# Performance work log

Hardware: AMD Instinct MI355X
Metric: run time of the kernel (lower is better)

Reference implementation:

```python
import jax, jax.numpy as jnp
import numpy as np

B, N, D, H, ND = 16, 512, 768, 12, 32
DK = D // H  # 64
GRID = 11    # hard-coded 11x11 patch grid in SpatialCirclePosition.patch


def setup_inputs() -> dict:
    key = jax.random.key(0)
    ks = jax.random.split(key, 10)
    features = jax.random.normal(ks[0], (B, N, D), dtype=jnp.float32)
    boxes = jax.random.uniform(ks[1], (B, N, 4), dtype=jnp.float32)  # normalized [0,1]
    sizes_wh = jax.random.randint(ks[2], (B, 2), 512, 1024).astype(jnp.int32)
    image_sizes = jnp.concatenate([sizes_wh, sizes_wh], axis=-1)  # (B,4) = [w,h,w,h]
    s = 0.02
    Wq = jax.random.normal(ks[3], (D, D), dtype=jnp.float32) * s
    Wk = jax.random.normal(ks[4], (D, D), dtype=jnp.float32) * s
    Wv = jax.random.normal(ks[5], (D, D), dtype=jnp.float32) * s
    Wo = jax.random.normal(ks[6], (D, D), dtype=jnp.float32) * s
    bq = jnp.zeros((D,), jnp.float32); bk = jnp.zeros((D,), jnp.float32)
    bv = jnp.zeros((D,), jnp.float32); bo = jnp.zeros((D,), jnp.float32)
    gamma = jnp.ones((D,), jnp.float32); beta = jnp.zeros((D,), jnp.float32)
    dist_emb = jax.random.normal(ks[7], (ND, H), dtype=jnp.float32) * s
    return {"features": features, "boxes": boxes, "image_sizes": image_sizes,
            "Wq": Wq, "bq": bq, "Wk": Wk, "bk": bk, "Wv": Wv, "bv": bv,
            "Wo": Wo, "bo": bo, "gamma": gamma, "beta": beta, "dist_emb": dist_emb}


def _patch_bins(boxes_norm, image_sizes):
    # boxes_norm: (B,N,4) in [0,1]; image_sizes: (B,4)=[w,h,w,h] int
    sizes_f = image_sizes.astype(jnp.float32)
    boxes = boxes_norm * sizes_f[:, None, :]                       # pixel boxes
    spa = jnp.floor_divide(sizes_f[:, :2], 11.0)                   # (B,2) size_per_area
    lb = jnp.arange(GRID, dtype=jnp.float32)                       # (11,)
    hb = lb + 1.0
    wlb = lb[None, :] * spa[:, 0:1]; whb = hb[None, :] * spa[:, 0:1]   # (B,11)
    hlb = lb[None, :] * spa[:, 1:2]; hhb = hb[None, :] * spa[:, 1:2]
    cx = jnp.floor_divide(boxes[..., 0] + boxes[..., 2], 2.0)      # (B,N)
    cy = jnp.floor_divide(boxes[..., 1] + boxes[..., 3], 2.0)
    mx = (wlb[:, None, :] <= cx[..., None]) & (cx[..., None] <= whb[:, None, :])  # (B,N,11)
    my = (hlb[:, None, :] <= cy[..., None]) & (cy[..., None] <= hhb[:, None, :])
    px = jnp.argmax(mx.astype(jnp.float32), axis=-1)               # (B,N) int
    py = jnp.argmax(my.astype(jnp.float32), axis=-1)
    return px.astype(jnp.float32), py.astype(jnp.float32)


def _dist_bins(boxes_norm, image_sizes):
    px, py = _patch_bins(boxes_norm, image_sizes)
    dx = px[:, None, :] - px[:, :, None]                           # (B,N,N)
    dy = py[:, None, :] - py[:, :, None]
    dist = jnp.sqrt(dx * dx + dy * dy) * 2.0
    return dist.astype(jnp.int32)                                  # truncation == .long()


def reference(features, boxes, image_sizes, Wq, bq, Wk, bk, Wv, bv, Wo, bo, gamma, beta, dist_emb):
    # LayerNorm(d_model), eps matches torch default 1e-5
    mu = jnp.mean(features, axis=-1, keepdims=True)
    var = jnp.mean(jnp.square(features - mu), axis=-1, keepdims=True)
    x = (features - mu) * jax.lax.rsqrt(var + 1e-5) * gamma + beta

    bins = _dist_bins(boxes, image_sizes)                          # (B,N,N) int32
    dist_bias = dist_emb[bins]                                     # (B,N,N,H)
    dist_bias = jnp.transpose(dist_bias, (0, 3, 1, 2))             # (B,H,N,N)

    bsz, nq, _ = x.shape
    q = (x @ Wq.T + bq).reshape(bsz, nq, H, DK).transpose(0, 2, 1, 3)  # (B,H,N,DK)
    k = (x @ Wk.T + bk).reshape(bsz, nq, H, DK).transpose(0, 2, 1, 3)
    v = (x @ Wv.T + bv).reshape(bsz, nq, H, DK).transpose(0, 2, 1, 3)

    att = jnp.einsum('bhqd,bhkd->bhqk', q, k) / np.sqrt(DK).astype(np.float32)
    att = jax.nn.softmax(att + dist_bias, axis=-1)                 # (B,H,N,N)
    out = jnp.einsum('bhqk,bhkd->bhqd', att, v)
    out = out.transpose(0, 2, 1, 3).reshape(bsz, nq, H * DK)
    out = out @ Wo.T + bo
    return out, att
```

## Files before the change

### kernel.cpp

```cpp
#include <hip/hip_runtime.h>
#include <hip/hip_bf16.h>

typedef unsigned char uchar;
typedef __attribute__((ext_vector_type(8))) short bf16x8;
typedef __attribute__((ext_vector_type(4))) float f32x4;

__device__ __forceinline__ unsigned short f2bf(float f) {
  union { float f; unsigned int u; } v; v.f = f;
  unsigned int u = v.u + 0x7fffu + ((v.u >> 16) & 1u);
  return (unsigned short)(u >> 16);
}

__device__ __forceinline__ void async_cp16(void* lds, const void* g) {
  __builtin_amdgcn_global_load_lds(
      (const __attribute__((address_space(1))) unsigned int*)g,
      (__attribute__((address_space(3))) unsigned int*)lds, 16, 0, 0);
}

__global__ void pxpy_kernel(const float* __restrict__ boxes, const int* __restrict__ isz,
                            float* __restrict__ px, float* __restrict__ py) {
  int idx = blockIdx.x * 256 + threadIdx.x;
  int b = idx >> 9;
  float w = (float)isz[b * 4 + 0];
  float h = (float)isz[b * 4 + 1];
  float b0 = boxes[idx * 4 + 0] * w;
  float b1 = boxes[idx * 4 + 1] * h;
  float b2 = boxes[idx * 4 + 2] * w;
  float b3 = boxes[idx * 4 + 3] * h;
  float spw = floorf(w / 11.0f);
  float sph = floorf(h / 11.0f);
  float cx = floorf((b0 + b2) * 0.5f);
  float cy = floorf((b1 + b3) * 0.5f);
  int pxi = 0, pyi = 0;
  bool fx = false, fy = false;
  for (int j = 0; j < 11; ++j) {
    float jf = (float)j;
    if (!fx && jf * spw <= cx && cx <= (jf + 1.0f) * spw) { pxi = j; fx = true; }
    if (!fy && jf * sph <= cy && cy <= (jf + 1.0f) * sph) { pyi = j; fy = true; }
  }
  px[idx] = (float)pxi;
  py[idx] = (float)pyi;
}

__global__ void bins_kernel(const float* __restrict__ px, const float* __restrict__ py,
                            uchar* __restrict__ bins) {
  int r = blockIdx.x;
  int j = threadIdx.x;
  int b = r >> 9;
  float pxq = px[r], pyq = py[r];
  float dx = px[b * 512 + j] - pxq;
  float dy = py[b * 512 + j] - pyq;
  float d = sqrtf(dx * dx + dy * dy) * 2.0f;
  bins[(size_t)r * 512 + j] = (uchar)(int)d;
}

__global__ __launch_bounds__(256) void ln_kernel(const float* __restrict__ f,
                                                 const float* __restrict__ gamma,
                                                 const float* __restrict__ beta,
                                                 unsigned short* __restrict__ x) {
  const int r = blockIdx.x;
  const int t = threadIdx.x;
  const float* row = f + (size_t)r * 768;
  float e0 = row[t], e1 = row[t + 256], e2 = row[t + 512];
  float s = e0 + e1 + e2;
#pragma unroll
  for (int off = 32; off > 0; off >>= 1) s += __shfl_down(s, off);
  __shared__ float red[4];
  const int wid = t >> 6;
  if ((t & 63) == 0) red[wid] = s;
  __syncthreads();
  float mean = (red[0] + red[1] + red[2] + red[3]) * (1.0f / 768.0f);
  __syncthreads();
  float d0 = e0 - mean, d1 = e1 - mean, d2 = e2 - mean;
  float v = d0 * d0 + d1 * d1 + d2 * d2;
#pragma unroll
  for (int off = 32; off > 0; off >>= 1) v += __shfl_down(v, off);
  if ((t & 63) == 0) red[wid] = v;
  __syncthreads();
  float var = (red[0] + red[1] + red[2] + red[3]) * (1.0f / 768.0f);
  float rs = rsqrtf(var + 1e-5f);
  x[(size_t)r * 768 + t]       = f2bf(d0 * rs * gamma[t] + beta[t]);
  x[(size_t)r * 768 + t + 256] = f2bf(d1 * rs * gamma[t + 256] + beta[t + 256]);
  x[(size_t)r * 768 + t + 512] = f2bf(d2 * rs * gamma[t + 512] + beta[t + 512]);
}

__global__ void wprep_kernel(const float* __restrict__ Wq, const float* __restrict__ Wk,
                             const float* __restrict__ Wv, const float* __restrict__ Wo,
                             const float* __restrict__ bq, const float* __restrict__ bk,
                             const float* __restrict__ bv,
                             unsigned short* __restrict__ wcat, unsigned short* __restrict__ wo,
                             float* __restrict__ bcat) {
  int idx = blockIdx.x * 256 + threadIdx.x;
  if (idx < 1769472) {
    int n = idx / 768, k = idx % 768;
    float v = (n < 768) ? Wq[n * 768 + k]
            : (n < 1536) ? Wk[(n - 768) * 768 + k]
                         : Wv[(n - 1536) * 768 + k];
    wcat[idx] = f2bf(v);
  } else {
    int j = idx - 1769472;
    wo[j] = f2bf(Wo[j]);
  }
  if (idx < 2304)
    bcat[idx] = (idx < 768) ? bq[idx] : (idx < 1536) ? bk[idx - 768] : bv[idx - 1536];
}

template <bool OUTF32>
__global__ __launch_bounds__(256) void gemm_bt(const unsigned short* __restrict__ A,
                                               const unsigned short* __restrict__ Bt,
                                               const float* __restrict__ bias,
                                               void* __restrict__ Cout, int K, int ldc) {
  __shared__ unsigned short a_lds[128 * 32];
  __shared__ unsigned short b_lds[128 * 32];
  const int m0 = blockIdx.x * 128, n0 = blockIdx.y * 128;
  const int tid = threadIdx.x;
  const int lane = tid & 63, wid = tid >> 6;
  const int ln = lane & 15, quad = lane >> 4;
  const int wm = (wid & 1) * 64, wn = (wid >> 1) * 64;
  f32x4 acc[16] = {};
  for (int k0 = 0; k0 < K; k0 += 32) {
    __syncthreads();
#pragma unroll
    for (int rep = 0; rep < 2; ++rep) {
      int c = rep * 256 + tid;
      int row = c >> 2, e0 = (c & 3) << 3;
      async_cp16(&a_lds[c * 8], A + (size_t)(m0 + row) * K + k0 + e0);
      async_cp16(&b_lds[c * 8], Bt + (size_t)(n0 + row) * K + k0 + e0);
    }
    __syncthreads();
    bf16x8 af[4], bfr[4];
#pragma unroll
    for (int i = 0; i < 4; ++i)
      af[i] = *(const bf16x8*)&a_lds[(wm + i * 16 + ln) * 32 + quad * 8];
#pragma unroll
    for (int j = 0; j < 4; ++j)
      bfr[j] = *(const bf16x8*)&b_lds[(wn + j * 16 + ln) * 32 + quad * 8];
#pragma unroll
    for (int i = 0; i < 4; ++i)
#pragma unroll
      for (int j = 0; j < 4; ++j)
        acc[i * 4 + j] = __builtin_amdgcn_mfma_f32_16x16x32_bf16(af[i], bfr[j], acc[i * 4 + j], 0, 0, 0);
  }
#pragma unroll
  for (int i = 0; i < 4; ++i)
#pragma unroll
    for (int j = 0; j < 4; ++j)
#pragma unroll
      for (int r = 0; r < 4; ++r) {
        int rr = m0 + wm + i * 16 + quad * 4 + r;
        int cc = n0 + wn + j * 16 + ln;
        float v = acc[i * 4 + j][r] + bias[cc];
        if (OUTF32) ((float*)Cout)[(size_t)rr * ldc + cc] = v;
        else ((unsigned short*)Cout)[(size_t)rr * ldc + cc] = f2bf(v);
      }
}

__global__ __launch_bounds__(256) void attn_scores(const unsigned short* __restrict__ qkv,
                                                   const uchar* __restrict__ bins,
                                                   const float* __restrict__ dist_emb,
                                                   float* __restrict__ att) {
  const int bidx = blockIdx.x;
  const int qt = bidx & 7;
  const int h = (bidx >> 3) % 12;
  const int b = bidx / 96;
  __shared__ unsigned short qs[64 * 72];
  __shared__ unsigned short ks[64 * 72];
  __shared__ float demb[32];
  const int tid = threadIdx.x;
  if (tid < 32) demb[tid] = dist_emb[tid * 12 + h];
#pragma unroll
  for (int rep = 0; rep < 2; ++rep) {
    int c = rep * 256 + tid;
    int i = c >> 3, e0 = (c & 7) * 8;
    *(uint4*)&qs[i * 72 + e0] =
        *(const uint4*)(qkv + (size_t)(b * 512 + qt * 64 + i) * 2304 + h * 64 + e0);
  }
  const int lane = tid & 63, wid = tid >> 6;
  const int ln = lane & 15, quad = lane >> 4;
  f32x4 acc[32] = {};
  __syncthreads();
  bf16x8 a0 = *(const bf16x8*)&qs[(wid * 16 + ln) * 72 + quad * 8];
  bf16x8 a1 = *(const bf16x8*)&qs[(wid * 16 + ln) * 72 + 32 + quad * 8];
#pragma unroll
  for (int kc = 0; kc < 8; ++kc) {
    __syncthreads();
#pragma unroll
    for (int rep = 0; rep < 2; ++rep) {
      int c = rep * 256 + tid;
      int i = c >> 3, e0 = (c & 7) * 8;
      *(uint4*)&ks[i * 72 + e0] =
          *(const uint4*)(qkv + (size_t)(b * 512 + kc * 64 + i) * 2304 + 768 + h * 64 + e0);
    }
    __syncthreads();
#pragma unroll
    for (int t = 0; t < 4; ++t) {
      bf16x8 b0 = *(const bf16x8*)&ks[(t * 16 + ln) * 72 + quad * 8];
      bf16x8 b1 = *(const bf16x8*)&ks[(t * 16 + ln) * 72 + 32 + quad * 8];
      acc[kc * 4 + t] = __builtin_amdgcn_mfma_f32_16x16x32_bf16(a0, b0, acc[kc * 4 + t], 0, 0, 0);
      acc[kc * 4 + t] = __builtin_amdgcn_mfma_f32_16x16x32_bf16(a1, b1, acc[kc * 4 + t], 0, 0, 0);
    }
  }
  const int brow0 = qt * 64 + wid * 16 + quad * 4;
  const uchar* binb = bins + (size_t)b * 512 * 512;
#pragma unroll
  for (int i = 0; i < 32; ++i) {
    int col = (i >> 2) * 64 + (i & 3) * 16 + ln;
#pragma unroll
    for (int r = 0; r < 4; ++r) {
      int bin = binb[(size_t)(brow0 + r) * 512 + col];
      acc[i][r] = acc[i][r] * 0.125f + demb[bin];
    }
  }
  float inv[4];
#pragma unroll
  for (int r = 0; r < 4; ++r) {
    float m = -1e30f;
#pragma unroll
    for (int i = 0; i < 32; ++i) m = fmaxf(m, acc[i][r]);
    m = fmaxf(m, __shfl_xor(m, 1));
    m = fmaxf(m, __shfl_xor(m, 2));
    m = fmaxf(m, __shfl_xor(m, 4));
    m = fmaxf(m, __shfl_xor(m, 8));
    float s = 0.f;
#pragma unroll
    for (int i = 0; i < 32; ++i) { float p = __expf(acc[i][r] - m); acc[i][r] = p; s += p; }
    s += __shfl_xor(s, 1); s += __shfl_xor(s, 2); s += __shfl_xor(s, 4); s += __shfl_xor(s, 8);
    inv[r] = 1.0f / s;
  }
  float* ob = att + (size_t)((b * 12 + h) * 512) * 512;
#pragma unroll
  for (int i = 0; i < 32; ++i) {
    int col = (i >> 2) * 64 + (i & 3) * 16 + ln;
#pragma unroll
    for (int r = 0; r < 4; ++r)
      ob[(size_t)(brow0 + r) * 512 + col] = acc[i][r] * inv[r];
  }
}

__global__ __launch_bounds__(256) void attn_pv(const float* __restrict__ att,
                                               const unsigned short* __restrict__ qkv,
                                               unsigned short* __restrict__ attnout) {
  const int bidx = blockIdx.x;
  const int qt2 = bidx & 3;
  const int h = (bidx >> 2) % 12;
  const int b = bidx / 48;
  __shared__ unsigned short as_[128 * 72];
  __shared__ unsigned short vt[64 * 72];
  const int tid = threadIdx.x;
  const int lane = tid & 63, wid = tid >> 6;
  const int ln = lane & 15, quad = lane >> 4;
  const float* ab = att + (size_t)((b * 12 + h) * 512) * 512;
  f32x4 acc[8] = {};
  for (int kc = 0; kc < 8; ++kc) {
    __syncthreads();
#pragma unroll
    for (int rep = 0; rep < 8; ++rep) {
      int c = rep * 256 + tid;
      int i = c >> 4, e0 = (c & 15) * 4;
      float4 f = *(const float4*)&ab[(size_t)(qt2 * 128 + i) * 512 + kc * 64 + e0];
      unsigned short u4[4] = {f2bf(f.x), f2bf(f.y), f2bf(f.z), f2bf(f.w)};
      *(uint2*)&as_[i * 72 + e0] = *(uint2*)u4;
    }
#pragma unroll
    for (int rep = 0; rep < 2; ++rep) {
      int c = rep * 256 + tid;
      int n = c >> 3, e0 = (c & 7) * 8;
      uint4 xv = *(const uint4*)(qkv + (size_t)(b * 512 + kc * 64 + n) * 2304 + 1536 + h * 64 + e0);
      const unsigned short* xs = (const unsigned short*)&xv;
#pragma unroll
      for (int j = 0; j < 8; ++j) vt[(e0 + j) * 72 + n] = xs[j];
    }
    __syncthreads();
    bf16x8 af[2][2];
#pragma unroll
    for (int rt = 0; rt < 2; ++rt)
#pragma unroll
      for (int kk = 0; kk < 2; ++kk)
        af[rt][kk] = *(const bf16x8*)&as_[(wid * 32 + rt * 16 + ln) * 72 + kk * 32 + quad * 8];
#pragma unroll
    for (int ct = 0; ct < 4; ++ct) {
#pragma unroll
      for (int kk = 0; kk < 2; ++kk) {
        bf16x8 bg = *(const bf16x8*)&vt[(ct * 16 + ln) * 72 + kk * 32 + quad * 8];
#pragma unroll
        for (int rt = 0; rt < 2; ++rt)
          acc[rt * 4 + ct] = __builtin_amdgcn_mfma_f32_16x16x32_bf16(af[rt][kk], bg, acc[rt * 4 + ct], 0, 0, 0);
      }
    }
  }
#pragma unroll
  for (int rt = 0; rt < 2; ++rt)
#pragma unroll
    for (int ct = 0; ct < 4; ++ct)
#pragma unroll
      for (int r = 0; r < 4; ++r) {
        int m = b * 512 + qt2 * 128 + wid * 32 + rt * 16 + quad * 4 + r;
        int cc = h * 64 + ct * 16 + ln;
        attnout[(size_t)m * 768 + cc] = f2bf(acc[rt * 4 + ct][r]);
      }
}

extern "C" void kernel_launch(void* const* d_in, const int* in_sizes, int n_in,
                              void* d_out, int out_size, void* d_ws, size_t ws_size,
                              hipStream_t stream) {
  const float* features = (const float*)d_in[0];
  const float* boxes    = (const float*)d_in[1];
  const int*   isz      = (const int*)d_in[2];
  const float* Wq = (const float*)d_in[3];
  const float* bq = (const float*)d_in[4];
  const float* Wk = (const float*)d_in[5];
  const float* bk = (const float*)d_in[6];
  const float* Wv = (const float*)d_in[7];
  const float* bv = (const float*)d_in[8];
  const float* Wo = (const float*)d_in[9];
  const float* bo = (const float*)d_in[10];
  const float* gamma = (const float*)d_in[11];
  const float* beta  = (const float*)d_in[12];
  const float* dist_emb = (const float*)d_in[13];

  float* out = (float*)d_out;
  float* att = out + (size_t)8192 * 768;

  char* w = (char*)d_ws;
  float* px = (float*)w;          w += 8192 * 4;
  float* py = (float*)w;          w += 8192 * 4;
  uchar* bins = (uchar*)w;        w += (size_t)16 * 512 * 512;
  unsigned short* x = (unsigned short*)w;       w += (size_t)8192 * 768 * 2;
  unsigned short* wcat = (unsigned short*)w;    w += (size_t)2304 * 768 * 2;
  unsigned short* wo = (unsigned short*)w;      w += (size_t)768 * 768 * 2;
  float* bcat = (float*)w;                      w += 2304 * 4;
  unsigned short* qkv = (unsigned short*)w;     w += (size_t)8192 * 2304 * 2;
  unsigned short* attnout = (unsigned short*)w; w += (size_t)8192 * 768 * 2;

  pxpy_kernel<<<32, 256, 0, stream>>>(boxes, isz, px, py);
  bins_kernel<<<8192, 512, 0, stream>>>(px, py, bins);
  ln_kernel<<<8192, 256, 0, stream>>>(features, gamma, beta, x);
  wprep_kernel<<<9216, 256, 0, stream>>>(Wq, Wk, Wv, Wo, bq, bk, bv, wcat, wo, bcat);
  gemm_bt<false><<<dim3(64, 18), 256, 0, stream>>>(x, wcat, bcat, qkv, 768, 2304);
  attn_scores<<<1536, 256, 0, stream>>>(qkv, bins, dist_emb, att);
  attn_pv<<<768, 256, 0, stream>>>(att, qkv, attnout);
  gemm_bt<true><<<dim3(64, 6), 256, 0, stream>>>(attnout, wo, bo, out, 768, 768);
}
```

Measured before the change: 469.8 us.

## Fuse attention scores/softmax with PV product to avoid re-reading att

Merges the score/softmax kernel and the P·V kernel into one. Normalized probabilities stay in registers, are converted to bf16 into LDS per 64-key chunk, and are multiplied with V loaded per chunk. This removes the second kernel's full fp32 re-read of the large attention matrix and one launch. The att output store becomes a nontemporal store. The cost is that each block reloads V for its own 64 query rows, with smaller blocks than the old 128-row tiling, and the fused kernel holds both the score accumulators and the output accumulators, so register pressure rises.

```diff
diff --git a/kernel.cpp b/kernel.cpp
--- a/kernel.cpp
+++ b/kernel.cpp
@@ -155,10 +155,11 @@
       }
 }
 
-__global__ __launch_bounds__(256) void attn_scores(const unsigned short* __restrict__ qkv,
-                                                   const uchar* __restrict__ bins,
-                                                   const float* __restrict__ dist_emb,
-                                                   float* __restrict__ att) {
+__global__ __launch_bounds__(256) void attn_fused(const unsigned short* __restrict__ qkv,
+                                                  const uchar* __restrict__ bins,
+                                                  const float* __restrict__ dist_emb,
+                                                  float* __restrict__ att,
+                                                  unsigned short* __restrict__ attnout) {
   const int bidx = blockIdx.x;
   const int qt = bidx & 7;
   const int h = (bidx >> 3) % 12;
@@ -227,40 +228,27 @@
     s += __shfl_xor(s, 1); s += __shfl_xor(s, 2); s += __shfl_xor(s, 4); s += __shfl_xor(s, 8);
     inv[r] = 1.0f / s;
   }
+#pragma unroll
+  for (int i = 0; i < 32; ++i)
+#pragma unroll
+    for (int r = 0; r < 4; ++r) acc[i][r] *= inv[(r)];
   float* ob = att + (size_t)((b * 12 + h) * 512) * 512;
 #pragma unroll
   for (int i = 0; i < 32; ++i) {
     int col = (i >> 2) * 64 + (i & 3) * 16 + ln;
 #pragma unroll
     for (int r = 0; r < 4; ++r)
-      ob[(size_t)(brow0 + r) * 512 + col] = acc[i][r] * inv[r];
-  }
-}
-
-__global__ __launch_bounds__(256) void attn_pv(const float* __restrict__ att,
-                                               const unsigned short* __restrict__ qkv,
-                                               unsigned short* __restrict__ attnout) {
-  const int bidx = blockIdx.x;
-  const int qt2 = bidx & 3;
-  const int h = (bidx >> 2) % 12;
-  const int b = bidx / 48;
-  __shared__ unsigned short as_[128 * 72];
-  __shared__ unsigned short vt[64 * 72];
-  const int tid = threadIdx.x;
-  const int lane = tid & 63, wid = tid >> 6;
-  const int ln = lane & 15, quad = lane >> 4;
-  const float* ab = att + (size_t)((b * 12 + h) * 512) * 512;
-  f32x4 acc[8] = {};
+      __builtin_nontemporal_store(acc[i][r], &ob[(size_t)(brow0 + r) * 512 + col]);
+  }
+  f32x4 acc_o[4] = {};
+#pragma unroll
   for (int kc = 0; kc < 8; ++kc) {
     __syncthreads();
 #pragma unroll
-    for (int rep = 0; rep < 8; ++rep) {
-      int c = rep * 256 + tid;
-      int i = c >> 4, e0 = (c & 15) * 4;
-      float4 f = *(const float4*)&ab[(size_t)(qt2 * 128 + i) * 512 + kc * 64 + e0];
-      unsigned short u4[4] = {f2bf(f.x), f2bf(f.y), f2bf(f.z), f2bf(f.w)};
-      *(uint2*)&as_[i * 72 + e0] = *(uint2*)u4;
-    }
+    for (int t = 0; t < 4; ++t)
+#pragma unroll
+      for (int r = 0; r < 4; ++r)
+        qs[(wid * 16 + quad * 4 + r) * 72 + t * 16 + ln] = f2bf(acc[kc * 4 + t][r]);
 #pragma unroll
     for (int rep = 0; rep < 2; ++rep) {
       int c = rep * 256 + tid;
@@ -268,36 +256,27 @@
       uint4 xv = *(const uint4*)(qkv + (size_t)(b * 512 + kc * 64 + n) * 2304 + 1536 + h * 64 + e0);
       const unsigned short* xs = (const unsigned short*)&xv;
 #pragma unroll
-      for (int j = 0; j < 8; ++j) vt[(e0 + j) * 72 + n] = xs[j];
-    }
-    __syncthreads();
-    bf16x8 af[2][2];
-#pragma unroll
-    for (int rt = 0; rt < 2; ++rt)
-#pragma unroll
-      for (int kk = 0; kk < 2; ++kk)
-        af[rt][kk] = *(const bf16x8*)&as_[(wid * 32 + rt * 16 + ln) * 72 + kk * 32 + quad * 8];
-#pragma unroll
-    for (int ct = 0; ct < 4; ++ct) {
-#pragma unroll
-      for (int kk = 0; kk < 2; ++kk) {
-        bf16x8 bg = *(const bf16x8*)&vt[(ct * 16 + ln) * 72 + kk * 32 + quad * 8];
-#pragma unroll
-        for (int rt = 0; rt < 2; ++rt)
-          acc[rt * 4 + ct] = __builtin_amdgcn_mfma_f32_16x16x32_bf16(af[rt][kk], bg, acc[rt * 4 + ct], 0, 0, 0);
+      for (int j = 0; j < 8; ++j) ks[(e0 + j) * 72 + n] = xs[j];
+    }
+    __syncthreads();
+#pragma unroll
+    for (int kk = 0; kk < 2; ++kk) {
+      bf16x8 af = *(const bf16x8*)&qs[(wid * 16 + ln) * 72 + kk * 32 + quad * 8];
+#pragma unroll
+      for (int ct = 0; ct < 4; ++ct) {
+        bf16x8 bg = *(const bf16x8*)&ks[(ct * 16 + ln) * 72 + kk * 32 + quad * 8];
+        acc_o[ct] = __builtin_amdgcn_mfma_f32_16x16x32_bf16(af, bg, acc_o[ct], 0, 0, 0);
       }
     }
   }
 #pragma unroll
-  for (int rt = 0; rt < 2; ++rt)
-#pragma unroll
-    for (int ct = 0; ct < 4; ++ct)
-#pragma unroll
-      for (int r = 0; r < 4; ++r) {
-        int m = b * 512 + qt2 * 128 + wid * 32 + rt * 16 + quad * 4 + r;
-        int cc = h * 64 + ct * 16 + ln;
-        attnout[(size_t)m * 768 + cc] = f2bf(acc[rt * 4 + ct][r]);
-      }
+  for (int ct = 0; ct < 4; ++ct)
+#pragma unroll
+    for (int r = 0; r < 4; ++r) {
+      int m = b * 512 + qt * 64 + wid * 16 + quad * 4 + r;
+      int cc = h * 64 + ct * 16 + ln;
+      attnout[(size_t)m * 768 + cc] = f2bf(acc_o[ct][r]);
+    }
 }
 
 extern "C" void kernel_launch(void* const* d_in, const int* in_sizes, int n_in,
@@ -337,7 +316,6 @@
   ln_kernel<<<8192, 256, 0, stream>>>(features, gamma, beta, x);
   wprep_kernel<<<9216, 256, 0, stream>>>(Wq, Wk, Wv, Wo, bq, bk, bv, wcat, wo, bcat);
   gemm_bt<false><<<dim3(64, 18), 256, 0, stream>>>(x, wcat, bcat, qkv, 768, 2304);
-  attn_scores<<<1536, 256, 0, stream>>>(qkv, bins, dist_emb, att);
-  attn_pv<<<768, 256, 0, stream>>>(att, qkv, attnout);
+  attn_fused<<<1536, 256, 0, stream>>>(qkv, bins, dist_emb, att, attnout);
   gemm_bt<true><<<dim3(64, 6), 256, 0, stream>>>(attnout, wo, bo, out, 768, 768);
 }
```

New measurement: 452.8 us. 3.6% less time.
